# Kernel tuning notes

Measured on AMD Instinct MI355X. Metric: run time of the kernel, lower is better.

Reference implementation:

```python
import jax, jax.numpy as jnp
import numpy as np

N = 50000
E = 800000
IN_CH = 512
OUT_CH = 64
ITERATIONS = 3  # adjacency power order; iterations-1 spmm steps


def setup_inputs() -> dict:
    key = jax.random.key(0)
    k1, k2, k3, k4, k5 = jax.random.split(key, 5)
    adj_indices = jax.random.randint(k1, (2, E), 0, N, dtype=jnp.int32)
    adj_values = jax.random.uniform(k2, (E,), dtype=jnp.float32)
    features = jax.random.normal(k3, (N, IN_CH), dtype=jnp.float32)
    # xavier-uniform init bounds
    bw = float(np.sqrt(6.0 / (IN_CH + OUT_CH)))
    weight = jax.random.uniform(k4, (IN_CH, OUT_CH), minval=-bw, maxval=bw, dtype=jnp.float32)
    bb = float(np.sqrt(6.0 / (1 + OUT_CH)))
    bias = jax.random.uniform(k5, (1, OUT_CH), minval=-bb, maxval=bb, dtype=jnp.float32)
    return {"adj_indices": adj_indices, "adj_values": adj_values,
            "features": features, "weight": weight, "bias": bias}


def reference(adj_indices, adj_values, features, weight, bias):
    # dense projection: [N, in] @ [in, out] -> [N, out]
    x = features @ weight
    # dropout is identity in eval mode (training=False)
    row, col = adj_indices[0], adj_indices[1]
    # (iterations - 1) sparse-dense matmuls: x <- A @ x
    for _ in range(ITERATIONS - 1):
        gathered = adj_values[:, None] * x[col]          # [E, out]
        x = jax.ops.segment_sum(gathered, row, num_segments=N)
    return x + bias
```

## Files before the change

### kernel.cpp

```cpp
#include <hip/hip_runtime.h>
#include <hip/hip_bf16.h>
#include <hip/hip_fp16.h>

#define NN 50000
#define INCH 512
#define OUTCH 64
#define NTILES 3125
#define MAXD 48
#define GB 782
#define SB 512
#define RPB 32
#define NBUCKET 1563
#define NPART 8
#define BCAPP 112
#define TSTR 16

typedef __attribute__((ext_vector_type(8))) short short8;
typedef __attribute__((ext_vector_type(4))) float floatx4;
typedef unsigned long long u64;

__device__ __forceinline__ unsigned packbf2(float a, float b) {
    __hip_bfloat162 h = __float22bfloat162_rn(make_float2(a, b));
    unsigned r;
    __builtin_memcpy(&r, &h, 4);
    return r;
}
__device__ __forceinline__ unsigned short f2bf(float f) {
    unsigned u = __float_as_uint(f);
    return (unsigned short)((u + 0x7FFFu + ((u >> 16) & 1u)) >> 16);
}
__device__ __forceinline__ float bf2f(unsigned short u) {
    return __uint_as_float(((unsigned)u) << 16);
}

__global__ __launch_bounds__(256) void prep_kernel(const float* __restrict__ W,
                                                   unsigned short* __restrict__ Wbf,
                                                   int* __restrict__ btail) {
    const int i = blockIdx.x * 256 + threadIdx.x;
    if (i < (NBUCKET * NPART * TSTR) / 4)
        *reinterpret_cast<uint4*>(btail + i * 4) = uint4{0u, 0u, 0u, 0u};
    if (i < INCH * OUTCH) {
        const int k = i >> 6;
        const int n = i & 63;
        Wbf[n * INCH + k] = f2bf(W[i]);
    }
}

__global__ __launch_bounds__(256, 4) void fused_gemm_scatter(
        const float* __restrict__ A, const unsigned short* __restrict__ Wbf,
        unsigned short* __restrict__ C,
        const int* __restrict__ rows, const int* __restrict__ cols,
        const float* __restrict__ vals, int* __restrict__ btail,
        u64* __restrict__ buckets, int E_) {
    __shared__ unsigned short ldsT[4][16 * 64];
    const int t = threadIdx.x;

    if (blockIdx.x >= GB) {
        const int s = blockIdx.x - GB;
        const int part = s & 7;
        for (int e = s * 256 + t; e < E_; e += SB * 256) {
            const int r = __builtin_nontemporal_load(rows + e);
            const int c = __builtin_nontemporal_load(cols + e);
            const float v = __builtin_nontemporal_load(vals + e);
            const unsigned short hv = __half_as_ushort(__float2half(v));
            const u64 rec = (u64)(unsigned)(r & 0xFFFF)
                          | ((u64)(unsigned)(c & 0xFFFF) << 16)
                          | ((u64)hv << 32);
            const int sb = (r >> 5) * NPART + part;
            const int pos = atomicAdd(&btail[sb * TSTR], 1);
            if (pos < BCAPP)
                buckets[(size_t)sb * BCAPP + pos] = rec;
        }
        return;
    }

    const int lane = t & 63;
    const int wave = t >> 6;
    const int tile = blockIdx.x * 4 + wave;
    if (tile >= NTILES) return;
    const int rbase = tile * 16;
    const int frow = lane & 15;
    const int quad = lane >> 4;
    const float* Ap = A + (size_t)(rbase + frow) * INCH + quad * 8;
    const unsigned short* Bp = Wbf + frow * INCH + quad * 8;

    floatx4 acc[4] = {floatx4{0,0,0,0}, floatx4{0,0,0,0}, floatx4{0,0,0,0}, floatx4{0,0,0,0}};

#pragma unroll
    for (int c = 0; c < 16; ++c) {
        const floatx4 a0 = __builtin_nontemporal_load((const floatx4*)(Ap + c * 32));
        const floatx4 a1 = __builtin_nontemporal_load((const floatx4*)(Ap + c * 32 + 4));
        short8 bfr[4];
#pragma unroll
        for (int f = 0; f < 4; ++f)
            bfr[f] = *(const short8*)(Bp + (size_t)f * 16 * INCH + c * 32);
        uint4 au;
        au.x = packbf2(a0[0], a0[1]);
        au.y = packbf2(a0[2], a0[3]);
        au.z = packbf2(a1[0], a1[1]);
        au.w = packbf2(a1[2], a1[3]);
        const short8 af = *(const short8*)&au;
#pragma unroll
        for (int f = 0; f < 4; ++f)
            acc[f] = __builtin_amdgcn_mfma_f32_16x16x32_bf16(af, bfr[f], acc[f], 0, 0, 0);
    }

    unsigned short* myT = ldsT[wave];
#pragma unroll
    for (int f = 0; f < 4; ++f)
#pragma unroll
        for (int reg = 0; reg < 4; ++reg)
            myT[(quad * 4 + reg) * 64 + f * 16 + frow] = f2bf(acc[f][reg]);
    unsigned short* Cw = C + (size_t)rbase * OUTCH;
#pragma unroll
    for (int it = 0; it < 2; ++it) {
        const short8 v = *(const short8*)&myT[it * 512 + lane * 8];
        __builtin_nontemporal_store(v, (short8*)(Cw + it * 512 + lane * 8));
    }
}

__global__ __launch_bounds__(256) void bucketize(
        const int* __restrict__ btail, const u64* __restrict__ buckets,
        unsigned* __restrict__ ell, int* __restrict__ deg) {
    __shared__ int cnt[RPB];
    __shared__ __align__(16) unsigned stage[RPB * MAXD];
    const int t = threadIdx.x;
    const int b = blockIdx.x;

    if (t < RPB) cnt[t] = 0;
    for (int j = t; j < RPB * MAXD; j += 256) stage[j] = 0u;
    __syncthreads();

    for (int part = 0; part < NPART; ++part) {
        const int sb = b * NPART + part;
        int n = btail[sb * TSTR];
        n = n < BCAPP ? n : BCAPP;
        const u64* base = buckets + (size_t)sb * BCAPP;
        for (int i = t; i < n; i += 256) {
            const u64 rec = base[i];
            const int rloc = (int)rec & 31;
            const int slot = atomicAdd(&cnt[rloc], 1);
            if (slot < MAXD)
                stage[rloc * MAXD + slot] = (unsigned)(rec >> 16);
        }
    }
    __syncthreads();

    uint4* dst = (uint4*)(ell + (size_t)b * RPB * MAXD);
    const uint4* src = (const uint4*)stage;
    for (int j = t; j < (RPB * MAXD) / 4; j += 256) dst[j] = src[j];
    const int row = b * RPB + t;
    if (t < RPB && row < NN) {
        int d = cnt[t];
        deg[row] = d < MAXD ? d : MAXD;
    }
}

template <bool LAST>
__global__ __launch_bounds__(256) void spmm_full(const int* __restrict__ deg,
                                                 const unsigned* __restrict__ ell,
                                                 const unsigned short* __restrict__ xin,
                                                 void* __restrict__ xout_,
                                                 const float* __restrict__ bias) {
    const int t = threadIdx.x;
    const int lane = t & 63;
    const int eslot = lane >> 3;
    const int cg = lane & 7;
    const int row = blockIdx.x * 4 + (t >> 6);
    int d = deg[row];
    d = d < MAXD ? d : MAXD;
    const unsigned* eb = ell + (size_t)row * MAXD;

    unsigned p[6];
#pragma unroll
    for (int j = 0; j < 6; ++j)
        p[j] = __builtin_nontemporal_load(eb + eslot + 8 * j);
#pragma unroll
    for (int j = 0; j < 6; ++j)
        if (eslot + 8 * j >= d) p[j] = 0u;

    const unsigned short* xh = xin + cg * 8;
    float acc[8] = {0.f, 0.f, 0.f, 0.f, 0.f, 0.f, 0.f, 0.f};

#pragma unroll
    for (int j = 0; j < 6; ++j) {
        if (d > 8 * j) {
            const unsigned P = p[j];
            const short8 xv = *(const short8*)(xh + (size_t)(P & 0xFFFFu) * OUTCH);
            const float v = __half2float(__ushort_as_half((unsigned short)(P >> 16)));
#pragma unroll
            for (int k = 0; k < 8; ++k)
                acc[k] = fmaf(v, bf2f((unsigned short)xv[k]), acc[k]);
        }
    }

#pragma unroll
    for (int k = 0; k < 8; ++k) {
        acc[k] += __shfl_xor(acc[k], 8, 64);
        acc[k] += __shfl_xor(acc[k], 16, 64);
        acc[k] += __shfl_xor(acc[k], 32, 64);
    }

    if (eslot == 0) {
        const int chb = cg * 8;
        if (LAST) {
            float* op = (float*)xout_ + (size_t)row * OUTCH + chb;
            const floatx4 b0 = *(const floatx4*)(bias + chb);
            const floatx4 b1 = *(const floatx4*)(bias + chb + 4);
            floatx4 o0, o1;
            o0[0] = acc[0] + b0[0]; o0[1] = acc[1] + b0[1];
            o0[2] = acc[2] + b0[2]; o0[3] = acc[3] + b0[3];
            o1[0] = acc[4] + b1[0]; o1[1] = acc[5] + b1[1];
            o1[2] = acc[6] + b1[2]; o1[3] = acc[7] + b1[3];
            __builtin_nontemporal_store(o0, (floatx4*)op);
            __builtin_nontemporal_store(o1, (floatx4*)(op + 4));
        } else {
            unsigned short* op = (unsigned short*)xout_ + (size_t)row * OUTCH + chb;
            short8 o;
#pragma unroll
            for (int k = 0; k < 8; ++k) o[k] = (short)f2bf(acc[k]);
            __builtin_nontemporal_store(o, (short8*)op);
        }
    }
}

extern "C" void kernel_launch(void* const* d_in, const int* in_sizes, int n_in,
                              void* d_out, int out_size, void* d_ws, size_t ws_size,
                              hipStream_t stream) {
    const int*   adj   = (const int*)d_in[0];
    const float* avals = (const float*)d_in[1];
    const float* feat  = (const float*)d_in[2];
    const float* W     = (const float*)d_in[3];
    const float* bias  = (const float*)d_in[4];
    float* out = (float*)d_out;

    const int E_ = in_sizes[1];
    const int* rows = adj;
    const int* cols = adj + E_;

    unsigned short* x0  = (unsigned short*)d_ws;
    unsigned short* x1  = x0 + (size_t)NN * OUTCH;
    unsigned short* Wbf = x1 + (size_t)NN * OUTCH;
    unsigned* ell = (unsigned*)(Wbf + (size_t)OUTCH * INCH);
    u64* buckets = (u64*)(ell + (size_t)NBUCKET * RPB * MAXD);
    int* btail = (int*)(buckets + (size_t)NBUCKET * NPART * BCAPP);
    int* deg = btail + NBUCKET * NPART * TSTR;

    prep_kernel<<<196, 256, 0, stream>>>(W, Wbf, btail);

    fused_gemm_scatter<<<GB + SB, 256, 0, stream>>>(feat, Wbf, x0, rows, cols, avals,
                                                    btail, buckets, E_);

    bucketize<<<NBUCKET, 256, 0, stream>>>(btail, buckets, ell, deg);

    spmm_full<false><<<NN / 4, 256, 0, stream>>>(deg, ell, x0, x1, nullptr);
    spmm_full<true><<<NN / 4, 256, 0, stream>>>(deg, ell, x1, out, bias);
}
```

Measured before the change: 259.0 us.

## Split fused GEMM/scatter into separate kernels and adjust cache hints

Splits the fused GEMM plus edge-scatter kernel into two launches, a GEMM kernel and a standalone scatter kernel with a larger grid of 1024 blocks. It also changes cache policy: the GEMM feature loads, the x0 stores and the intermediate spmm stores become ordinary cached accesses, while the bucketize record reads become nontemporal. The aim is to avoid contention between the two workloads and to let the spmm passes hit the just-written bf16 data in cache. The cost is one extra kernel launch and the loss of overlap between GEMM and scatter.

```diff
diff --git a/kernel.cpp b/kernel.cpp
--- a/kernel.cpp
+++ b/kernel.cpp
@@ -8,7 +8,7 @@
 #define NTILES 3125
 #define MAXD 48
 #define GB 782
-#define SB 512
+#define SCB 1024
 #define RPB 32
 #define NBUCKET 1563
 #define NPART 8
@@ -46,34 +46,11 @@
     }
 }
 
-__global__ __launch_bounds__(256, 4) void fused_gemm_scatter(
+__global__ __launch_bounds__(256, 4) void gemm_kernel(
         const float* __restrict__ A, const unsigned short* __restrict__ Wbf,
-        unsigned short* __restrict__ C,
-        const int* __restrict__ rows, const int* __restrict__ cols,
-        const float* __restrict__ vals, int* __restrict__ btail,
-        u64* __restrict__ buckets, int E_) {
+        unsigned short* __restrict__ C) {
     __shared__ unsigned short ldsT[4][16 * 64];
     const int t = threadIdx.x;
-
-    if (blockIdx.x >= GB) {
-        const int s = blockIdx.x - GB;
-        const int part = s & 7;
-        for (int e = s * 256 + t; e < E_; e += SB * 256) {
-            const int r = __builtin_nontemporal_load(rows + e);
-            const int c = __builtin_nontemporal_load(cols + e);
-            const float v = __builtin_nontemporal_load(vals + e);
-            const unsigned short hv = __half_as_ushort(__float2half(v));
-            const u64 rec = (u64)(unsigned)(r & 0xFFFF)
-                          | ((u64)(unsigned)(c & 0xFFFF) << 16)
-                          | ((u64)hv << 32);
-            const int sb = (r >> 5) * NPART + part;
-            const int pos = atomicAdd(&btail[sb * TSTR], 1);
-            if (pos < BCAPP)
-                buckets[(size_t)sb * BCAPP + pos] = rec;
-        }
-        return;
-    }
-
     const int lane = t & 63;
     const int wave = t >> 6;
     const int tile = blockIdx.x * 4 + wave;
@@ -88,17 +65,17 @@
 
 #pragma unroll
     for (int c = 0; c < 16; ++c) {
-        const floatx4 a0 = __builtin_nontemporal_load((const floatx4*)(Ap + c * 32));
-        const floatx4 a1 = __builtin_nontemporal_load((const floatx4*)(Ap + c * 32 + 4));
+        const float4 a0 = *(const float4*)(Ap + c * 32);
+        const float4 a1 = *(const float4*)(Ap + c * 32 + 4);
         short8 bfr[4];
 #pragma unroll
         for (int f = 0; f < 4; ++f)
             bfr[f] = *(const short8*)(Bp + (size_t)f * 16 * INCH + c * 32);
         uint4 au;
-        au.x = packbf2(a0[0], a0[1]);
-        au.y = packbf2(a0[2], a0[3]);
-        au.z = packbf2(a1[0], a1[1]);
-        au.w = packbf2(a1[2], a1[3]);
+        au.x = packbf2(a0.x, a0.y);
+        au.y = packbf2(a0.z, a0.w);
+        au.z = packbf2(a1.x, a1.y);
+        au.w = packbf2(a1.z, a1.w);
         const short8 af = *(const short8*)&au;
 #pragma unroll
         for (int f = 0; f < 4; ++f)
@@ -115,7 +92,27 @@
 #pragma unroll
     for (int it = 0; it < 2; ++it) {
         const short8 v = *(const short8*)&myT[it * 512 + lane * 8];
-        __builtin_nontemporal_store(v, (short8*)(Cw + it * 512 + lane * 8));
+        *(short8*)(Cw + it * 512 + lane * 8) = v;
+    }
+}
+
+__global__ __launch_bounds__(256) void scatter_kernel(
+        const int* __restrict__ rows, const int* __restrict__ cols,
+        const float* __restrict__ vals, int* __restrict__ btail,
+        u64* __restrict__ buckets, int E_) {
+    const int part = blockIdx.x & 7;
+    for (int e = blockIdx.x * 256 + threadIdx.x; e < E_; e += SCB * 256) {
+        const int r = __builtin_nontemporal_load(rows + e);
+        const int c = __builtin_nontemporal_load(cols + e);
+        const float v = __builtin_nontemporal_load(vals + e);
+        const unsigned short hv = __half_as_ushort(__float2half(v));
+        const u64 rec = (u64)(unsigned)(r & 0xFFFF)
+                      | ((u64)(unsigned)(c & 0xFFFF) << 16)
+                      | ((u64)hv << 32);
+        const int sb = (r >> 5) * NPART + part;
+        const int pos = atomicAdd(&btail[sb * TSTR], 1);
+        if (pos < BCAPP)
+            buckets[(size_t)sb * BCAPP + pos] = rec;
     }
 }
 
@@ -137,7 +134,7 @@
         n = n < BCAPP ? n : BCAPP;
         const u64* base = buckets + (size_t)sb * BCAPP;
         for (int i = t; i < n; i += 256) {
-            const u64 rec = base[i];
+            const u64 rec = __builtin_nontemporal_load(base + i);
             const int rloc = (int)rec & 31;
             const int slot = atomicAdd(&cnt[rloc], 1);
             if (slot < MAXD)
@@ -219,7 +216,7 @@
             short8 o;
 #pragma unroll
             for (int k = 0; k < 8; ++k) o[k] = (short)f2bf(acc[k]);
-            __builtin_nontemporal_store(o, (short8*)op);
+            *(short8*)op = o;
         }
     }
 }
@@ -248,8 +245,9 @@
 
     prep_kernel<<<196, 256, 0, stream>>>(W, Wbf, btail);
 
-    fused_gemm_scatter<<<GB + SB, 256, 0, stream>>>(feat, Wbf, x0, rows, cols, avals,
-                                                    btail, buckets, E_);
+    gemm_kernel<<<GB, 256, 0, stream>>>(feat, Wbf, x0);
+
+    scatter_kernel<<<SCB, 256, 0, stream>>>(rows, cols, avals, btail, buckets, E_);
 
     bucketize<<<NBUCKET, 256, 0, stream>>>(btail, buckets, ell, deg);
 
```

Measured after the change: 266.6 us. 2.9% more time.
